# Kernel tuning notes

Hardware: AMD Instinct MI355X
Metric: run time of the kernel (lower is better)

The kernel has to match this reference:

```python
import jax, jax.numpy as jnp
import numpy as np

T, B, I, H = 1024, 128, 512, 512
KEEP_PROB = 0.7  # dropout = 0.3


def setup_inputs() -> dict:
    key = jax.random.key(0)
    ks = jax.random.split(key, 8)
    xs = jax.random.normal(ks[0], (T, B, I), dtype=jnp.float32)
    s_in = 1.0 / np.sqrt(I)
    s_h = 1.0 / np.sqrt(H)
    W_ih1 = jax.random.normal(ks[1], (4 * H, I), dtype=jnp.float32) * s_in
    W_hh1 = jax.random.normal(ks[2], (4 * H, H), dtype=jnp.float32) * s_h
    W_ih2 = jax.random.normal(ks[3], (4 * H, H), dtype=jnp.float32) * s_h
    W_hh2 = jax.random.normal(ks[4], (4 * H, H), dtype=jnp.float32) * s_h
    b_ih1 = jnp.zeros((4 * H,), jnp.float32)
    b_hh1 = jnp.zeros((4 * H,), jnp.float32)
    b_ih2 = jnp.zeros((4 * H,), jnp.float32)
    b_hh2 = jnp.zeros((4 * H,), jnp.float32)
    # recurrent dropout mask: same Bernoulli(keep_prob) 0/1 mask for the whole sequence
    mask = jax.random.bernoulli(ks[5], KEEP_PROB, (B, H)).astype(jnp.float32)
    return {"xs": xs, "W_ih1": W_ih1, "W_hh1": W_hh1, "b_ih1": b_ih1, "b_hh1": b_hh1,
            "W_ih2": W_ih2, "W_hh2": W_hh2, "b_ih2": b_ih2, "b_hh2": b_hh2, "mask": mask}


def _lstm_cell(x, h, c, W_ih, W_hh, b_ih, b_hh):
    # PyTorch nn.LSTMCell: gates ordered (i, f, g, o)
    gates = x @ W_ih.T + b_ih + h @ W_hh.T + b_hh  # [B, 4H]
    i, f, g, o = jnp.split(gates, 4, axis=-1)
    c_new = jax.nn.sigmoid(f) * c + jax.nn.sigmoid(i) * jnp.tanh(g)
    h_new = jax.nn.sigmoid(o) * jnp.tanh(c_new)
    return h_new, c_new


def reference(xs, W_ih1, W_hh1, b_ih1, b_hh1, W_ih2, W_hh2, b_ih2, b_hh2, mask):
    drop = mask * (1.0 / KEEP_PROB)  # [B, H]; applied to both h and c (training mode)

    def step(carry, x):
        h1, c1, h2, c2 = carry
        h1, c1 = _lstm_cell(x, h1, c1, W_ih1, W_hh1, b_ih1, b_hh1)
        h1, c1 = h1 * drop, c1 * drop
        h2, c2 = _lstm_cell(h1, h2, c2, W_ih2, W_hh2, b_ih2, b_hh2)
        h2, c2 = h2 * drop, c2 * drop
        return (h1, c1, h2, c2), h2

    z = jnp.zeros((xs.shape[1], W_hh1.shape[1]), xs.dtype)
    init = (z, z, z, z)
    _, hs = jax.lax.scan(step, init, xs)
    return hs  # [T, B, H]
```

## Files before the change

kernel.cpp:

```cpp
#include <hip/hip_runtime.h>
#include <stdint.h>
#include <stddef.h>

typedef unsigned short ushort_t;
typedef __attribute__((ext_vector_type(8))) short short8;
typedef __attribute__((ext_vector_type(4))) float floatx4;

#define T_STEPS 1024
#define BATCH   128
#define HID     512
#define NBLK    256
#define NTHR    256
#define INV_KEEP 1.4285714285714286f

__device__ unsigned g_sync[384];

struct Params {
  const float* xs;
  const float* Wih1; const float* Whh1; const float* bih1; const float* bhh1;
  const float* Wih2; const float* Whh2; const float* bih2; const float* bhh2;
  const float* mask;
  float* out;
  char* ws;
};

__device__ __forceinline__ void gridbar(unsigned gen) {
  __syncthreads();
  const int bid = blockIdx.x;
  if (bid == 0) {
    if (threadIdx.x < 64) {
      if (threadIdx.x == 0) {
        __threadfence();
        __hip_atomic_store(&g_sync[64 + 0], gen, __ATOMIC_RELAXED,
                           __HIP_MEMORY_SCOPE_AGENT);
      }
      const int base = 64 + (int)threadIdx.x * 4;
      for (;;) {
        bool ok = true;
#pragma unroll
        for (int k = 0; k < 4; ++k)
          ok &= (__hip_atomic_load(&g_sync[base + k], __ATOMIC_RELAXED,
                                   __HIP_MEMORY_SCOPE_AGENT) >= gen);
        if (__all(ok)) break;
        __builtin_amdgcn_s_sleep(1);
      }
      if (threadIdx.x == 0) {
        __threadfence();
        __hip_atomic_store(&g_sync[32], gen, __ATOMIC_RELEASE,
                           __HIP_MEMORY_SCOPE_AGENT);
      }
    }
  } else {
    if (threadIdx.x == 0) {
      __threadfence();
      __hip_atomic_store(&g_sync[64 + bid], gen, __ATOMIC_RELAXED,
                         __HIP_MEMORY_SCOPE_AGENT);
      while (__hip_atomic_load(&g_sync[32], __ATOMIC_RELAXED,
                               __HIP_MEMORY_SCOPE_AGENT) < gen)
        __builtin_amdgcn_s_sleep(1);
      __threadfence();
    }
  }
  __syncthreads();
}

__device__ __forceinline__ ushort_t f2b(float a) {
  unsigned u = __float_as_uint(a);
  u += 0x7FFFu + ((u >> 16) & 1u);
  return (ushort_t)(u >> 16);
}

__global__ __launch_bounds__(NTHR, 1) void lstm_persist(Params p) {
  extern __shared__ ushort_t Wl[];

  char* ws = p.ws;
  auto H1HI = [&](int par) { return (ushort_t*)(ws + 524288 + par * 262144); };
  auto H1LO = [&](int par) { return (ushort_t*)(ws + 524288 + par * 262144 + 131072); };
  auto H2HI = [&](int par) { return (ushort_t*)(ws + 1048576 + par * 262144); };
  auto H2LO = [&](int par) { return (ushort_t*)(ws + 1048576 + par * 262144 + 131072); };
  auto XSHI = [&](int par) { return (ushort_t*)(ws + 1572864 + par * 262144); };
  auto XSLO = [&](int par) { return (ushort_t*)(ws + 1572864 + par * 262144 + 131072); };

  const int bid = blockIdx.x, tid = threadIdx.x;
  const int gtid = bid * NTHR + tid;
  const int layer = bid >> 7;
  const int c8 = (bid & 127) >> 1;
  const int bhalf = bid & 1;
  const int lane = tid & 63, w = tid >> 6;
  const int jj = lane & 15, quad = lane >> 4;
  const int rbase = bhalf * 64 + w * 16;

  const float* Wih = layer ? p.Wih2 : p.Wih1;
  const float* Whh = layer ? p.Whh2 : p.Whh1;
  const float* bih = layer ? p.bih2 : p.bih1;
  const float* bhh = layer ? p.bhh2 : p.bhh1;

  for (int i = tid; i < 32768; i += NTHR) {
    int e = i & 7, jjw = (i >> 3) & 15, ntw = (i >> 7) & 1, kg = i >> 8;
    int k = kg * 8 + e;
    int col = ((jjw >> 2) << 9) + c8 * 8 + ntw * 4 + (jjw & 3);
    float wv = (k < 512) ? Wih[col * 512 + k] : Whh[col * 512 + (k - 512)];
    unsigned uw = __float_as_uint(wv);
    Wl[i] = (ushort_t)(uw >> 16);
    float wf = __uint_as_float(uw & 0xFFFF0000u);
    Wl[32768 + i] = f2b(wv - wf);
  }
  {
    uint4 zz = {0u, 0u, 0u, 0u};
    uint4* dst = (uint4*)(ws + 524288);
    for (int i = gtid; i < 65536; i += NBLK * NTHR) dst[i] = zz;
  }
  {
    float v = p.xs[gtid];
    unsigned uv = __float_as_uint(v);
    XSHI(0)[gtid] = (ushort_t)(uv >> 16);
    float hf = __uint_as_float(uv & 0xFFFF0000u);
    XSLO(0)[gtid] = f2b(v - hf);
  }
  float bsum[2];
#pragma unroll
  for (int nt = 0; nt < 2; ++nt) {
    int colW = ((jj >> 2) << 9) + c8 * 8 + nt * 4 + (jj & 3);
    bsum[nt] = bih[colW] + bhh[colW];
  }
  float dpre[2][4];
  float creg[2][4];
#pragma unroll
  for (int nt = 0; nt < 2; ++nt)
#pragma unroll
    for (int e = 0; e < 4; ++e) {
      int r = rbase + quad * 4 + e;
      int hgc = c8 * 8 + nt * 4 + (lane & 3);
      dpre[nt][e] = p.mask[r * 512 + hgc] * INV_KEEP;
      creg[nt][e] = 0.f;
    }

  unsigned gen = 1;
  gridbar(gen++);

  const int rowbyte = ((rbase + jj) * 512 + quad * 8) * 2;

#pragma unroll 1
  for (unsigned u = 0; u <= T_STEPS; ++u) {
    if (u <= T_STEPS - 2) {
      float v = p.xs[(size_t)(u + 1) * 65536 + gtid];
      unsigned uv = __float_as_uint(v);
      int pn = (u + 1) & 1;
      XSHI(pn)[gtid] = (ushort_t)(uv >> 16);
      float hf = __uint_as_float(uv & 0xFFFF0000u);
      XSLO(pn)[gtid] = f2b(v - hf);
    }

    const bool active = layer ? (u >= 1) : (u < T_STEPS);
    if (active) {
      const int t = layer ? (int)u - 1 : (int)u;
      const int pu = (int)u & 1, pv = pu ^ 1;
      const ushort_t *aLoHi, *aLoLo, *aHiHi, *aHiLo;
      ushort_t *whHi, *whLo;
      if (layer == 0) {
        aLoHi = XSHI(pu); aLoLo = XSLO(pu);
        aHiHi = H1HI(pv); aHiLo = H1LO(pv);
        whHi = H1HI(pu);  whLo = H1LO(pu);
      } else {
        aLoHi = H1HI(pv); aLoLo = H1LO(pv);
        aHiHi = H2HI(pu); aHiLo = H2LO(pu);
        whHi = H2HI(pv);  whLo = H2LO(pv);
      }

      floatx4 acc[2];
      acc[0] = (floatx4){bsum[0], bsum[0], bsum[0], bsum[0]};
      acc[1] = (floatx4){bsum[1], bsum[1], bsum[1], bsum[1]};

      auto ldchunk = [&](int c, uint4* dst) {
        const char* bh = (const char*)((c < 8) ? aLoHi : aHiHi);
        const char* bl = (const char*)((c < 8) ? aLoLo : aHiLo);
        int kb = (c & 7) * 128;
#pragma unroll
        for (int ks = 0; ks < 2; ++ks) {
          int off = rowbyte + kb + ks * 64;
          dst[ks * 2 + 0] = *(const uint4*)(bh + off);
          dst[ks * 2 + 1] = *(const uint4*)(bl + off);
        }
      };

      uint4 ring[4][4];
      ldchunk(0, ring[0]);
      ldchunk(1, ring[1]);
      ldchunk(2, ring[2]);
#pragma unroll
      for (int c = 0; c < 16; ++c) {
        if (c < 13) ldchunk(c + 3, ring[(c + 3) & 3]);
        uint4* cur = ring[c & 3];
#pragma unroll
        for (int ks = 0; ks < 2; ++ks) {
          short8 ahf = *(const short8*)&cur[ks * 2 + 0];
          short8 alf = *(const short8*)&cur[ks * 2 + 1];
#pragma unroll
          for (int nt = 0; nt < 2; ++nt) {
            int o = (((c * 8 + ks * 4 + quad) * 2 + nt) * 16 + jj) * 8;
            short8 bhf = *(const short8*)&Wl[o];
            short8 blf = *(const short8*)&Wl[32768 + o];
            acc[nt] = __builtin_amdgcn_mfma_f32_16x16x32_bf16(ahf, bhf, acc[nt], 0, 0, 0);
            acc[nt] = __builtin_amdgcn_mfma_f32_16x16x32_bf16(ahf, blf, acc[nt], 0, 0, 0);
            acc[nt] = __builtin_amdgcn_mfma_f32_16x16x32_bf16(alf, bhf, acc[nt], 0, 0, 0);
          }
        }
      }

      const int sb = (lane & 48) | (lane & 3);
#pragma unroll
      for (int nt = 0; nt < 2; ++nt)
#pragma unroll
        for (int e = 0; e < 4; ++e) {
          float v = acc[nt][e];
          float gi = __shfl(v, sb + 0, 64);
          float gf = __shfl(v, sb + 4, 64);
          float gg = __shfl(v, sb + 8, 64);
          float go = __shfl(v, sb + 12, 64);
          float si = 1.f / (1.f + __expf(-gi));
          float sf = 1.f / (1.f + __expf(-gf));
          float so = 1.f / (1.f + __expf(-go));
          float tg = 2.f / (1.f + __expf(-2.f * gg)) - 1.f;
          int r = rbase + quad * 4 + e;
          int hgc = c8 * 8 + nt * 4 + (lane & 3);
          int ci = r * 512 + hgc;
          float cn = sf * creg[nt][e] + si * tg;
          float tc = 2.f / (1.f + __expf(-2.f * cn)) - 1.f;
          float hn = so * tc;
          float d = dpre[nt][e];
          hn *= d; cn *= d;
          creg[nt][e] = cn;
          unsigned uh = __float_as_uint(hn);
          whHi[ci] = (ushort_t)(uh >> 16);
          float hf = __uint_as_float(uh & 0xFFFF0000u);
          whLo[ci] = f2b(hn - hf);
          if (layer) p.out[(size_t)t * 65536 + ci] = hn;
        }
    }
    if (u < T_STEPS) gridbar(gen++);
  }
}

extern "C" void kernel_launch(void* const* d_in, const int* in_sizes, int n_in,
                              void* d_out, int out_size, void* d_ws, size_t ws_size,
                              hipStream_t stream) {
  (void)in_sizes; (void)n_in; (void)out_size; (void)ws_size;
  Params p;
  p.xs   = (const float*)d_in[0];
  p.Wih1 = (const float*)d_in[1];
  p.Whh1 = (const float*)d_in[2];
  p.bih1 = (const float*)d_in[3];
  p.bhh1 = (const float*)d_in[4];
  p.Wih2 = (const float*)d_in[5];
  p.Whh2 = (const float*)d_in[6];
  p.bih2 = (const float*)d_in[7];
  p.bhh2 = (const float*)d_in[8];
  p.mask = (const float*)d_in[9];
  p.out  = (float*)d_out;
  p.ws   = (char*)d_ws;

  static bool attr_done = false;
  if (!attr_done) {
    (void)hipFuncSetAttribute(reinterpret_cast<const void*>(lstm_persist),
                              hipFuncAttributeMaxDynamicSharedMemorySize, 131072);
    attr_done = true;
  }

  void* sym = nullptr;
  hipGetSymbolAddress(&sym, HIP_SYMBOL(g_sync));
  hipMemsetAsync(sym, 0, 384 * sizeof(unsigned), stream);

  void* args[] = { &p };
  hipLaunchCooperativeKernel(reinterpret_cast<void*>(lstm_persist),
                             dim3(NBLK), dim3(NTHR), args, 131072, stream);
}
```

Before: 28.41 ms.

## Replace centralized grid barrier with decentralized per-block flags and fewer larger blocks

Halves the block count to 128 with 512 threads each, so each block covers the full batch for one column group. The old master/worker grid barrier is replaced by per-block generation flags on padded cache lines: every block publishes its own counter and polls all the others directly, and the next xs load is issued before the wait. This removes the extra hop through a master block and the serialized release, at the cost of more polling traffic. It also restricts h stores to the lanes that hold distinct values, avoiding redundant writes.

```diff
diff --git a/kernel.cpp b/kernel.cpp
--- a/kernel.cpp
+++ b/kernel.cpp
@@ -9,11 +9,11 @@
 #define T_STEPS 1024
 #define BATCH   128
 #define HID     512
-#define NBLK    256
-#define NTHR    256
+#define NBLK    128
+#define NTHR    512
 #define INV_KEEP 1.4285714285714286f
 
-__device__ unsigned g_sync[384];
+__device__ unsigned g_sync[4096];
 
 struct Params {
   const float* xs;
@@ -24,44 +24,29 @@
   char* ws;
 };
 
-__device__ __forceinline__ void gridbar(unsigned gen) {
+__device__ __forceinline__ void waitgen(unsigned target) {
+  if (threadIdx.x < 64) {
+    const int l = threadIdx.x;
+    for (;;) {
+      unsigned a = __hip_atomic_load(&g_sync[l * 32], __ATOMIC_RELAXED,
+                                     __HIP_MEMORY_SCOPE_AGENT);
+      unsigned b = __hip_atomic_load(&g_sync[(l + 64) * 32], __ATOMIC_RELAXED,
+                                     __HIP_MEMORY_SCOPE_AGENT);
+      if (__all(a >= target && b >= target)) break;
+      __builtin_amdgcn_s_sleep(1);
+    }
+    __threadfence();
+  }
   __syncthreads();
-  const int bid = blockIdx.x;
-  if (bid == 0) {
-    if (threadIdx.x < 64) {
-      if (threadIdx.x == 0) {
-        __threadfence();
-        __hip_atomic_store(&g_sync[64 + 0], gen, __ATOMIC_RELAXED,
-                           __HIP_MEMORY_SCOPE_AGENT);
-      }
-      const int base = 64 + (int)threadIdx.x * 4;
-      for (;;) {
-        bool ok = true;
-#pragma unroll
-        for (int k = 0; k < 4; ++k)
-          ok &= (__hip_atomic_load(&g_sync[base + k], __ATOMIC_RELAXED,
-                                   __HIP_MEMORY_SCOPE_AGENT) >= gen);
-        if (__all(ok)) break;
-        __builtin_amdgcn_s_sleep(1);
-      }
-      if (threadIdx.x == 0) {
-        __threadfence();
-        __hip_atomic_store(&g_sync[32], gen, __ATOMIC_RELEASE,
-                           __HIP_MEMORY_SCOPE_AGENT);
-      }
-    }
-  } else {
-    if (threadIdx.x == 0) {
-      __threadfence();
-      __hip_atomic_store(&g_sync[64 + bid], gen, __ATOMIC_RELAXED,
-                         __HIP_MEMORY_SCOPE_AGENT);
-      while (__hip_atomic_load(&g_sync[32], __ATOMIC_RELAXED,
-                               __HIP_MEMORY_SCOPE_AGENT) < gen)
-        __builtin_amdgcn_s_sleep(1);
-      __threadfence();
-    }
-  }
+}
+
+__device__ __forceinline__ void postgen(unsigned value) {
   __syncthreads();
+  if (threadIdx.x == 0) {
+    __threadfence();
+    __hip_atomic_store(&g_sync[blockIdx.x * 32], value, __ATOMIC_RELAXED,
+                       __HIP_MEMORY_SCOPE_AGENT);
+  }
 }
 
 __device__ __forceinline__ ushort_t f2b(float a) {
@@ -83,12 +68,11 @@
 
   const int bid = blockIdx.x, tid = threadIdx.x;
   const int gtid = bid * NTHR + tid;
-  const int layer = bid >> 7;
-  const int c8 = (bid & 127) >> 1;
-  const int bhalf = bid & 1;
+  const int layer = bid >> 6;
+  const int c8 = bid & 63;
   const int lane = tid & 63, w = tid >> 6;
   const int jj = lane & 15, quad = lane >> 4;
-  const int rbase = bhalf * 64 + w * 16;
+  const int rbase = w * 16;
 
   const float* Wih = layer ? p.Wih2 : p.Wih1;
   const float* Whh = layer ? p.Whh2 : p.Whh1;
@@ -135,20 +119,25 @@
       creg[nt][e] = 0.f;
     }
 
-  unsigned gen = 1;
-  gridbar(gen++);
+  postgen(1);
 
   const int rowbyte = ((rbase + jj) * 512 + quad * 8) * 2;
+  const bool dostore = (jj < 4);
 
 #pragma unroll 1
   for (unsigned u = 0; u <= T_STEPS; ++u) {
-    if (u <= T_STEPS - 2) {
-      float v = p.xs[(size_t)(u + 1) * 65536 + gtid];
-      unsigned uv = __float_as_uint(v);
+    const bool havex = (u + 2 <= T_STEPS);
+    float xv = 0.f;
+    if (havex) xv = p.xs[(size_t)(u + 1) * 65536 + gtid];
+
+    waitgen(u + 1);
+
+    if (havex) {
+      unsigned uv = __float_as_uint(xv);
       int pn = (u + 1) & 1;
       XSHI(pn)[gtid] = (ushort_t)(uv >> 16);
       float hf = __uint_as_float(uv & 0xFFFF0000u);
-      XSLO(pn)[gtid] = f2b(v - hf);
+      XSLO(pn)[gtid] = f2b(xv - hf);
     }
 
     const bool active = layer ? (u >= 1) : (u < T_STEPS);
@@ -230,14 +219,16 @@
           float d = dpre[nt][e];
           hn *= d; cn *= d;
           creg[nt][e] = cn;
-          unsigned uh = __float_as_uint(hn);
-          whHi[ci] = (ushort_t)(uh >> 16);
-          float hf = __uint_as_float(uh & 0xFFFF0000u);
-          whLo[ci] = f2b(hn - hf);
-          if (layer) p.out[(size_t)t * 65536 + ci] = hn;
+          if (dostore) {
+            unsigned uh = __float_as_uint(hn);
+            whHi[ci] = (ushort_t)(uh >> 16);
+            float hf = __uint_as_float(uh & 0xFFFF0000u);
+            whLo[ci] = f2b(hn - hf);
+            if (layer) p.out[(size_t)t * 65536 + ci] = hn;
+          }
         }
     }
-    if (u < T_STEPS) gridbar(gen++);
+    if (u < T_STEPS) postgen(u + 2);
   }
 }
 
@@ -268,7 +259,7 @@
 
   void* sym = nullptr;
   hipGetSymbolAddress(&sym, HIP_SYMBOL(g_sync));
-  hipMemsetAsync(sym, 0, 384 * sizeof(unsigned), stream);
+  hipMemsetAsync(sym, 0, 4096 * sizeof(unsigned), stream);
 
   void* args[] = { &p };
   hipLaunchCooperativeKernel(reinterpret_cast<void*>(lstm_persist),
```

Measured after the change: 28.52 ms. About the same (+0.4%).
